# Kernel tuning notes

Measured on AMD Instinct MI355X. Metric: run time of the kernel, lower is better.

The kernel has to match this reference:

```python
import math
import jax, jax.numpy as jnp
import numpy as np

EMB_DIM = 1024
CFG_N_HEADS = 16
# Faithful to the torch module: n_heads collapses to 1 when config.n_heads < emb_dim
N_HEADS = CFG_N_HEADS if CFG_N_HEADS >= EMB_DIM else 1


def setup_inputs() -> dict:
    key = jax.random.key(0)
    ks = jax.random.split(key, 11)
    B, T, C = 4, 2048, EMB_DIM
    s = 1.0 / math.sqrt(C)
    return {
        "q": jax.random.normal(ks[0], (B, T, C), jnp.float32),
        "k": jax.random.normal(ks[1], (B, T, C), jnp.float32),
        "v": jax.random.normal(ks[2], (B, T, C), jnp.float32),
        "Wq": jax.random.normal(ks[3], (C, C), jnp.float32) * s,
        "bq": jax.random.normal(ks[4], (C,), jnp.float32) * s,
        "Wk": jax.random.normal(ks[5], (C, C), jnp.float32) * s,
        "bk": jax.random.normal(ks[6], (C,), jnp.float32) * s,
        "Wv": jax.random.normal(ks[7], (C, C), jnp.float32) * s,
        "bv": jax.random.normal(ks[8], (C,), jnp.float32) * s,
        "Wff": jax.random.normal(ks[9], (C, C), jnp.float32) * s,
        "bff": jax.random.normal(ks[10], (C,), jnp.float32) * s,
    }


def reference(q, k, v, Wq, bq, Wk, bk, Wv, bv, Wff, bff):
    B, T, C = q.shape
    H = N_HEADS
    D = C // H  # head dim (== C here since H degenerates to 1)
    # torch Linear: x @ W.T + b
    qp = (q @ Wq.T + bq).reshape(B, T, H, D).transpose(0, 2, 1, 3)  # [B,H,T,D]
    kp = (k @ Wk.T + bk).reshape(B, T, H, D).transpose(0, 2, 1, 3)
    vp = (v @ Wv.T + bv).reshape(B, T, H, D).transpose(0, 2, 1, 3)
    scale = 1.0 / math.sqrt(D)
    scores = jnp.einsum('bhqd,bhkd->bhqk', qp, kp) * scale  # [B,H,T,T]
    causal = jnp.tril(jnp.ones((T, T), dtype=bool))
    scores = jnp.where(causal[None, None, :, :], scores, -jnp.inf)
    attn = jax.nn.softmax(scores, axis=-1)
    out = jnp.einsum('bhqk,bhkd->bhqd', attn, vp)  # [B,H,T,D]
    out = out.transpose(0, 2, 1, 3).reshape(B, T, C)
    return out @ Wff.T + bff
```

## Files before the change

kernel.cpp:

```cpp
#include <hip/hip_runtime.h>
#include <stdint.h>

typedef unsigned short u16;
typedef short v8s __attribute__((ext_vector_type(8)));
typedef float v4f __attribute__((ext_vector_type(4)));

#define BM 128
#define BN 128
#define BK 32

__device__ __forceinline__ float b2f(u16 b) {
  union { unsigned u; float f; } x; x.u = ((unsigned)b) << 16; return x.f;
}
__device__ __forceinline__ u16 f2b(float f) {
  union { float f; unsigned u; } x; x.f = f;
  unsigned r = x.u + 0x7fffu + ((x.u >> 16) & 1u);
  return (u16)(r >> 16);
}

__device__ __forceinline__ void async_copy16(const void* g, void* lds) {
  __builtin_amdgcn_global_load_lds(
      (const __attribute__((address_space(1))) void*)g,
      (__attribute__((address_space(3))) void*)(uint32_t)(uintptr_t)lds,
      16, 0, 0);
}

__device__ __forceinline__ void xcd_swz(int& bx, int& by) {
  const int gx = gridDim.x;
  const int nwg = gx * gridDim.y;
  const int ord = blockIdx.y * gx + blockIdx.x;
  const int q = nwg >> 3, r = nwg & 7;
  const int xcd = ord & 7, local = ord >> 3;
  const int base = xcd < r ? xcd * (q + 1) : r * (q + 1) + (xcd - r) * q;
  const int s = base + local;
  bx = s % gx;
  by = s / gx;
}

__global__ __launch_bounds__(256) void cvt3_kernel(
    const float* __restrict__ i0, const float* __restrict__ i1,
    const float* __restrict__ i2, u16* __restrict__ o0, u16* __restrict__ o1,
    u16* __restrict__ o2, int n) {
  const int z = blockIdx.y;
  const float* in = z == 0 ? i0 : (z == 1 ? i1 : i2);
  u16* out = z == 0 ? o0 : (z == 1 ? o1 : o2);
  const int i = (blockIdx.x * 256 + threadIdx.x) * 8;
  if (i >= n) return;
  v4f a = *(const v4f*)(in + i);
  v4f b = *(const v4f*)(in + i + 4);
  v8s o;
#pragma unroll
  for (int j = 0; j < 4; j++) o[j] = (short)f2b(a[j]);
#pragma unroll
  for (int j = 0; j < 4; j++) o[4 + j] = (short)f2b(b[j]);
  *(v8s*)(out + i) = o;
}

__global__ __launch_bounds__(256) void cvt4_kernel(
    const float* __restrict__ i0, const float* __restrict__ i1,
    const float* __restrict__ i2, const float* __restrict__ i3,
    u16* __restrict__ o0, u16* __restrict__ o1, u16* __restrict__ o2,
    u16* __restrict__ o3, int n) {
  const int z = blockIdx.y;
  const float* in = z == 0 ? i0 : (z == 1 ? i1 : (z == 2 ? i2 : i3));
  u16* out = z == 0 ? o0 : (z == 1 ? o1 : (z == 2 ? o2 : o3));
  const int i = (blockIdx.x * 256 + threadIdx.x) * 8;
  if (i >= n) return;
  v4f a = *(const v4f*)(in + i);
  v4f b = *(const v4f*)(in + i + 4);
  v8s o;
#pragma unroll
  for (int j = 0; j < 4; j++) o[j] = (short)f2b(a[j]);
#pragma unroll
  for (int j = 0; j < 4; j++) o[4 + j] = (short)f2b(b[j]);
  *(v8s*)(out + i) = o;
}

template <bool HAS_BIAS, bool CAUSAL_K, bool OUT_F32>
__device__ __forceinline__ void gemm_body(
    const u16* __restrict__ A, int lda, const u16* __restrict__ Bm, int ldb,
    void* __restrict__ Cout_, int ldc, long cbase,
    const float* __restrict__ bias, int K, int m0, int n0) {
  __shared__ u16 ldsA[BM * BK];
  __shared__ u16 ldsB[BN * BK];

  const int tid = threadIdx.x;
  const int wave = tid >> 6, lane = tid & 63;
  const int wm = (wave >> 1) * 64, wn = (wave & 1) * 64;
  const int lrow = lane & 15, quad = lane >> 4;

  v4f acc[4][4];
#pragma unroll
  for (int i = 0; i < 4; i++)
#pragma unroll
    for (int j = 0; j < 4; j++) acc[i][j] = v4f{0.f, 0.f, 0.f, 0.f};

  int Keff = K;
  if (CAUSAL_K) {
    int ke = m0 + BM;
    Keff = ke < K ? ke : K;
  }

  const int r0 = tid >> 2;
  const int c0 = (tid & 3) * 8;
  const u16* pA0 = A + (long)(m0 + r0) * lda + c0;
  const u16* pA1 = A + (long)(m0 + 64 + r0) * lda + c0;
  const u16* pB0 = Bm + (long)(n0 + r0) * ldb + c0;
  const u16* pB1 = Bm + (long)(n0 + 64 + r0) * ldb + c0;
  u16* dA0 = ldsA + wave * 512;
  u16* dA1 = ldsA + 2048 + wave * 512;
  u16* dB0 = ldsB + wave * 512;
  u16* dB1 = ldsB + 2048 + wave * 512;

  for (int k0 = 0; k0 < Keff; k0 += BK) {
    async_copy16(pA0 + k0, dA0);
    async_copy16(pA1 + k0, dA1);
    async_copy16(pB0 + k0, dB0);
    async_copy16(pB1 + k0, dB1);
    __syncthreads();

    v8s af[4], bfr[4];
#pragma unroll
    for (int mt = 0; mt < 4; mt++)
      af[mt] = *(const v8s*)&ldsA[(wm + mt * 16 + lrow) * BK + quad * 8];
#pragma unroll
    for (int nt = 0; nt < 4; nt++)
      bfr[nt] = *(const v8s*)&ldsB[(wn + nt * 16 + lrow) * BK + quad * 8];
#pragma unroll
    for (int mt = 0; mt < 4; mt++)
#pragma unroll
      for (int nt = 0; nt < 4; nt++)
        acc[mt][nt] = __builtin_amdgcn_mfma_f32_16x16x32_bf16(
            af[mt], bfr[nt], acc[mt][nt], 0, 0, 0);
    __syncthreads();
  }

#pragma unroll
  for (int mt = 0; mt < 4; mt++) {
    const int rowBase = m0 + wm + mt * 16 + quad * 4;
#pragma unroll
    for (int nt = 0; nt < 4; nt++) {
      const int col = n0 + wn + nt * 16 + lrow;
      float bv = 0.f;
      if (HAS_BIAS) bv = bias[col];
#pragma unroll
      for (int i = 0; i < 4; i++) {
        const long idx = cbase + (long)(rowBase + i) * ldc + col;
        const float val = acc[mt][nt][i] + bv;
        if (OUT_F32)
          ((float*)Cout_)[idx] = val;
        else
          ((u16*)Cout_)[idx] = f2b(val);
      }
    }
  }
}

__global__ __launch_bounds__(256, 4) void qkv_gemm_kernel(
    const u16* __restrict__ a0, const u16* __restrict__ a1,
    const u16* __restrict__ a2, const u16* __restrict__ w0,
    const u16* __restrict__ w1, const u16* __restrict__ w2,
    const float* __restrict__ b0, const float* __restrict__ b1,
    const float* __restrict__ b2, u16* __restrict__ c0, u16* __restrict__ c1,
    u16* __restrict__ c2, int C) {
  const int z = blockIdx.z;
  const u16* A = z == 0 ? a0 : (z == 1 ? a1 : a2);
  const u16* W = z == 0 ? w0 : (z == 1 ? w1 : w2);
  const float* bias = z == 0 ? b0 : (z == 1 ? b1 : b2);
  u16* Cp = z == 0 ? c0 : (z == 1 ? c1 : c2);
  int bx, by;
  xcd_swz(bx, by);
  gemm_body<true, false, false>(A, C, W, C, Cp, C, 0,
                                bias, C, by * BM, bx * BN);
}

template <bool HAS_BIAS, bool CAUSAL_SKIP, bool CAUSAL_K, bool OUT_F32>
__global__ __launch_bounds__(256, 4) void gemm_bt_kernel(
    const u16* __restrict__ A, int lda, long sA,
    const u16* __restrict__ Bm, int ldb, long sB,
    void* __restrict__ Cout_, int ldc, long sC,
    const float* __restrict__ bias, int K) {
  int bx, by;
  xcd_swz(bx, by);
  const int m0 = by * BM;
  const int n0 = bx * BN;
  if (CAUSAL_SKIP && n0 > m0) return;
  const int z = blockIdx.z;
  gemm_body<HAS_BIAS, CAUSAL_K, OUT_F32>(
      A + (long)z * sA, lda, Bm + (long)z * sB, ldb, Cout_, ldc,
      (long)z * sC, bias, K, m0, n0);
}

__global__ __launch_bounds__(256) void transpose_kernel(
    const u16* __restrict__ in, u16* __restrict__ out) {
  __shared__ u16 tile[64][72];
  const int b = blockIdx.z;
  const int d0 = blockIdx.x * 64;
  const int t0 = blockIdx.y * 64;
  const u16* ip = in + (long)b * 2048 * 1024;
  u16* op = out + (long)b * 1024 * 2048;
  const int tid = threadIdx.x;
  const int tl = tid >> 2;
  const int dl = (tid & 3) * 16;
  const u16* src = ip + (long)(t0 + tl) * 1024 + d0 + dl;
  *(v8s*)&tile[tl][dl] = *(const v8s*)src;
  *(v8s*)&tile[tl][dl + 8] = *(const v8s*)(src + 8);
  __syncthreads();
  const int dd = tid >> 2;
  const int tt = (tid & 3) * 16;
  u16* dst = op + (long)(d0 + dd) * 2048 + t0 + tt;
  v8s o0, o1;
#pragma unroll
  for (int j = 0; j < 8; j++) o0[j] = (short)tile[tt + j][dd];
#pragma unroll
  for (int j = 0; j < 8; j++) o1[j] = (short)tile[tt + 8 + j][dd];
  *(v8s*)dst = o0;
  *(v8s*)(dst + 8) = o1;
}

__global__ __launch_bounds__(256) void softmax_kernel(u16* __restrict__ S) {
  const float scale = 0.03125f;
  const int i = blockIdx.x, b = blockIdx.y;
  const int tid = threadIdx.x;
  u16* row = S + ((long)b * 2048 + (long)i) * 2048;
  const int jb = tid * 8;
  const int Lw = ((i >> 7) + 1) << 7;
  v8s raw = {0, 0, 0, 0, 0, 0, 0, 0};
  if (jb <= i) raw = *(const v8s*)&row[jb];
  float v[8];
  float m = -1e30f;
#pragma unroll
  for (int jj = 0; jj < 8; jj++) {
    float x = (jb + jj <= i) ? b2f((u16)raw[jj]) * scale : -1e30f;
    v[jj] = x;
    m = fmaxf(m, x);
  }
#pragma unroll
  for (int off = 32; off; off >>= 1) m = fmaxf(m, __shfl_xor(m, off));
  __shared__ float red[4], red2[4];
  const int wave = tid >> 6, lane = tid & 63;
  if (lane == 0) red[wave] = m;
  __syncthreads();
  m = fmaxf(fmaxf(red[0], red[1]), fmaxf(red[2], red[3]));
  float s = 0.f, p[8];
#pragma unroll
  for (int jj = 0; jj < 8; jj++) {
    float e = (v[jj] > -1e29f) ? __expf(v[jj] - m) : 0.f;
    p[jj] = e;
    s += e;
  }
#pragma unroll
  for (int off = 32; off; off >>= 1) s += __shfl_xor(s, off);
  if (lane == 0) red2[wave] = s;
  __syncthreads();
  s = red2[0] + red2[1] + red2[2] + red2[3];
  const float inv = 1.0f / s;
  v8s outv;
#pragma unroll
  for (int jj = 0; jj < 8; jj++) outv[jj] = (short)f2b(p[jj] * inv);
  if (jb < Lw) *(v8s*)&row[jb] = outv;
}

extern "C" void kernel_launch(void* const* d_in, const int* in_sizes, int n_in,
                              void* d_out, int out_size, void* d_ws,
                              size_t ws_size, hipStream_t stream) {
  const float* q = (const float*)d_in[0];
  const float* k = (const float*)d_in[1];
  const float* v = (const float*)d_in[2];
  const float* Wq = (const float*)d_in[3];
  const float* bq = (const float*)d_in[4];
  const float* Wk = (const float*)d_in[5];
  const float* bk = (const float*)d_in[6];
  const float* Wv = (const float*)d_in[7];
  const float* bv = (const float*)d_in[8];
  const float* Wff = (const float*)d_in[9];
  const float* bff = (const float*)d_in[10];
  float* out = (float*)d_out;

  const int B = 4, T = 2048, C = 1024, M = B * T;
  const size_t MC = (size_t)M * C;
  const size_t CC = (size_t)C * C;
  u16* ws = (u16*)d_ws;
  u16* qb = ws;
  u16* kb = qb + MC;
  u16* vb = kb + MC;
  u16* Wqb = vb + MC;
  u16* Wkb = Wqb + CC;
  u16* Wvb = Wkb + CC;
  u16* Wffb = Wvb + CC;
  u16* Qp = Wffb + CC;
  u16* Kp = Qp + MC;
  u16* Vp = Kp + MC;
  u16* VpT = Vp + MC;
  u16* S = qb;
  u16* attn = Vp;

  dim3 blk(256);
  cvt3_kernel<<<dim3((int)(MC / 2048), 3), blk, 0, stream>>>(
      q, k, v, qb, kb, vb, (int)MC);
  cvt4_kernel<<<dim3((int)(CC / 2048), 4), blk, 0, stream>>>(
      Wq, Wk, Wv, Wff, Wqb, Wkb, Wvb, Wffb, (int)CC);

  qkv_gemm_kernel<<<dim3(C / BN, M / BM, 3), blk, 0, stream>>>(
      qb, kb, vb, Wqb, Wkb, Wvb, bq, bk, bv, Qp, Kp, Vp, C);
  transpose_kernel<<<dim3(C / 64, T / 64, B), blk, 0, stream>>>(Vp, VpT);
  gemm_bt_kernel<false, true, false, false>
      <<<dim3(T / BN, T / BM, B), blk, 0, stream>>>(
          Qp, C, (long)T * C, Kp, C, (long)T * C, S, T, (long)T * T,
          nullptr, C);
  softmax_kernel<<<dim3(T, B), blk, 0, stream>>>(S);
  gemm_bt_kernel<false, false, true, false>
      <<<dim3(C / BN, T / BM, B), blk, 0, stream>>>(
          S, T, (long)T * T, VpT, T, (long)C * T, attn, C, (long)T * C,
          nullptr, T);
  gemm_bt_kernel<true, false, false, true>
      <<<dim3(C / BN, M / BM, 1), blk, 0, stream>>>(
          attn, C, 0, Wffb, C, 0, out, C, 0, bff, C);
}
```

Measured before the change: 366.2 us.

## Double GEMM K-tile with XOR-swizzled LDS, pair causal tiles, wave-per-row softmax

Raises the GEMM K-tile from 32 to 64. The async global-to-LDS loads and the fragment reads now use an XOR-swizzled chunk layout, which halves the number of barriers per K and avoids LDS bank conflicts. The causal attention GEMMs get a block-order mapping that pairs short and long causal row blocks, to balance work across the GPU's compute dies (XCDs). Softmax now processes one row per wave instead of one per block, removing the shared-memory reductions and block barriers. The larger tile doubles LDS use per block, which may lower occupancy.

```diff
diff --git a/kernel.cpp b/kernel.cpp
--- a/kernel.cpp
+++ b/kernel.cpp
@@ -7,7 +7,7 @@
 
 #define BM 128
 #define BN 128
-#define BK 32
+#define BK 64
 
 __device__ __forceinline__ float b2f(u16 b) {
   union { unsigned u; float f; } x; x.u = ((unsigned)b) << 16; return x.f;
@@ -35,6 +35,15 @@
   const int s = base + local;
   bx = s % gx;
   by = s / gx;
+}
+
+__device__ __forceinline__ void causal_pair_swz(int& bx, int& by) {
+  const int gx = gridDim.x;
+  const int ord = blockIdx.y * gx + blockIdx.x;
+  const int k = ord & 7;
+  const int j = ord >> 3;
+  by = (j < gx) ? k : 15 - k;
+  bx = (j < gx) ? j : j - gx;
 }
 
 __global__ __launch_bounds__(256) void cvt3_kernel(
@@ -101,37 +110,43 @@
     Keff = ke < K ? ke : K;
   }
 
-  const int r0 = tid >> 2;
-  const int c0 = (tid & 3) * 8;
-  const u16* pA0 = A + (long)(m0 + r0) * lda + c0;
-  const u16* pA1 = A + (long)(m0 + 64 + r0) * lda + c0;
-  const u16* pB0 = Bm + (long)(n0 + r0) * ldb + c0;
-  const u16* pB1 = Bm + (long)(n0 + 64 + r0) * ldb + c0;
-  u16* dA0 = ldsA + wave * 512;
-  u16* dA1 = ldsA + 2048 + wave * 512;
-  u16* dB0 = ldsB + wave * 512;
-  u16* dB1 = ldsB + 2048 + wave * 512;
+  const int rA = lane >> 3;
+  const int uch = (lane & 7) ^ rA;
+  const u16* pA = A + (long)(m0 + wave * 8 + rA) * lda + uch * 8;
+  const u16* pB = Bm + (long)(n0 + wave * 8 + rA) * ldb + uch * 8;
+  u16* dA = ldsA + (wave * 8) * BK;
+  u16* dB = ldsB + (wave * 8) * BK;
 
   for (int k0 = 0; k0 < Keff; k0 += BK) {
-    async_copy16(pA0 + k0, dA0);
-    async_copy16(pA1 + k0, dA1);
-    async_copy16(pB0 + k0, dB0);
-    async_copy16(pB1 + k0, dB1);
+#pragma unroll
+    for (int c = 0; c < 4; c++) {
+      async_copy16(pA + (long)c * 32 * lda + k0, dA + c * 32 * BK);
+      async_copy16(pB + (long)c * 32 * ldb + k0, dB + c * 32 * BK);
+    }
     __syncthreads();
 
-    v8s af[4], bfr[4];
-#pragma unroll
-    for (int mt = 0; mt < 4; mt++)
-      af[mt] = *(const v8s*)&ldsA[(wm + mt * 16 + lrow) * BK + quad * 8];
-#pragma unroll
-    for (int nt = 0; nt < 4; nt++)
-      bfr[nt] = *(const v8s*)&ldsB[(wn + nt * 16 + lrow) * BK + quad * 8];
-#pragma unroll
-    for (int mt = 0; mt < 4; mt++)
-#pragma unroll
-      for (int nt = 0; nt < 4; nt++)
-        acc[mt][nt] = __builtin_amdgcn_mfma_f32_16x16x32_bf16(
-            af[mt], bfr[nt], acc[mt][nt], 0, 0, 0);
+#pragma unroll
+    for (int ks = 0; ks < 2; ks++) {
+      v8s af[4], bfr[4];
+#pragma unroll
+      for (int mt = 0; mt < 4; mt++) {
+        const int r = wm + mt * 16 + lrow;
+        af[mt] =
+            *(const v8s*)&ldsA[r * BK + ((ks * 4 + quad) ^ (r & 7)) * 8];
+      }
+#pragma unroll
+      for (int nt = 0; nt < 4; nt++) {
+        const int r = wn + nt * 16 + lrow;
+        bfr[nt] =
+            *(const v8s*)&ldsB[r * BK + ((ks * 4 + quad) ^ (r & 7)) * 8];
+      }
+#pragma unroll
+      for (int mt = 0; mt < 4; mt++)
+#pragma unroll
+        for (int nt = 0; nt < 4; nt++)
+          acc[mt][nt] = __builtin_amdgcn_mfma_f32_16x16x32_bf16(
+              af[mt], bfr[nt], acc[mt][nt], 0, 0, 0);
+    }
     __syncthreads();
   }
 
@@ -174,14 +189,18 @@
                                 bias, C, by * BM, bx * BN);
 }
 
-template <bool HAS_BIAS, bool CAUSAL_SKIP, bool CAUSAL_K, bool OUT_F32>
+template <bool HAS_BIAS, bool CAUSAL_SKIP, bool CAUSAL_K, bool OUT_F32,
+          int SWZ>
 __global__ __launch_bounds__(256, 4) void gemm_bt_kernel(
     const u16* __restrict__ A, int lda, long sA,
     const u16* __restrict__ Bm, int ldb, long sB,
     void* __restrict__ Cout_, int ldc, long sC,
     const float* __restrict__ bias, int K) {
   int bx, by;
-  xcd_swz(bx, by);
+  if (SWZ == 1)
+    causal_pair_swz(bx, by);
+  else
+    xcd_swz(bx, by);
   const int m0 = by * BM;
   const int n0 = bx * BN;
   if (CAUSAL_SKIP && n0 > m0) return;
@@ -220,45 +239,48 @@
 
 __global__ __launch_bounds__(256) void softmax_kernel(u16* __restrict__ S) {
   const float scale = 0.03125f;
-  const int i = blockIdx.x, b = blockIdx.y;
-  const int tid = threadIdx.x;
+  const int wave = threadIdx.x >> 6, lane = threadIdx.x & 63;
+  const int i = blockIdx.x * 4 + wave, b = blockIdx.y;
   u16* row = S + ((long)b * 2048 + (long)i) * 2048;
-  const int jb = tid * 8;
   const int Lw = ((i >> 7) + 1) << 7;
-  v8s raw = {0, 0, 0, 0, 0, 0, 0, 0};
-  if (jb <= i) raw = *(const v8s*)&row[jb];
-  float v[8];
+  float v[32];
   float m = -1e30f;
 #pragma unroll
-  for (int jj = 0; jj < 8; jj++) {
-    float x = (jb + jj <= i) ? b2f((u16)raw[jj]) * scale : -1e30f;
-    v[jj] = x;
-    m = fmaxf(m, x);
+  for (int c = 0; c < 4; c++) {
+    const int jb = c * 512 + lane * 8;
+    v8s raw = {0, 0, 0, 0, 0, 0, 0, 0};
+    if (jb <= i) raw = *(const v8s*)&row[jb];
+#pragma unroll
+    for (int jj = 0; jj < 8; jj++) {
+      float x = (jb + jj <= i) ? b2f((u16)raw[jj]) * scale : -1e30f;
+      v[c * 8 + jj] = x;
+      m = fmaxf(m, x);
+    }
   }
 #pragma unroll
   for (int off = 32; off; off >>= 1) m = fmaxf(m, __shfl_xor(m, off));
-  __shared__ float red[4], red2[4];
-  const int wave = tid >> 6, lane = tid & 63;
-  if (lane == 0) red[wave] = m;
-  __syncthreads();
-  m = fmaxf(fmaxf(red[0], red[1]), fmaxf(red[2], red[3]));
-  float s = 0.f, p[8];
-#pragma unroll
-  for (int jj = 0; jj < 8; jj++) {
-    float e = (v[jj] > -1e29f) ? __expf(v[jj] - m) : 0.f;
-    p[jj] = e;
-    s += e;
-  }
+  float s = 0.f;
+#pragma unroll
+  for (int c = 0; c < 4; c++)
+#pragma unroll
+    for (int jj = 0; jj < 8; jj++) {
+      float e = (v[c * 8 + jj] > -1e29f) ? __expf(v[c * 8 + jj] - m) : 0.f;
+      v[c * 8 + jj] = e;
+      s += e;
+    }
 #pragma unroll
   for (int off = 32; off; off >>= 1) s += __shfl_xor(s, off);
-  if (lane == 0) red2[wave] = s;
-  __syncthreads();
-  s = red2[0] + red2[1] + red2[2] + red2[3];
   const float inv = 1.0f / s;
-  v8s outv;
-#pragma unroll
-  for (int jj = 0; jj < 8; jj++) outv[jj] = (short)f2b(p[jj] * inv);
-  if (jb < Lw) *(v8s*)&row[jb] = outv;
+#pragma unroll
+  for (int c = 0; c < 4; c++) {
+    const int jb = c * 512 + lane * 8;
+    if (jb < Lw) {
+      v8s o;
+#pragma unroll
+      for (int jj = 0; jj < 8; jj++) o[jj] = (short)f2b(v[c * 8 + jj] * inv);
+      *(v8s*)&row[jb] = o;
+    }
+  }
 }
 
 extern "C" void kernel_launch(void* const* d_in, const int* in_sizes, int n_in,
@@ -304,16 +326,16 @@
   qkv_gemm_kernel<<<dim3(C / BN, M / BM, 3), blk, 0, stream>>>(
       qb, kb, vb, Wqb, Wkb, Wvb, bq, bk, bv, Qp, Kp, Vp, C);
   transpose_kernel<<<dim3(C / 64, T / 64, B), blk, 0, stream>>>(Vp, VpT);
-  gemm_bt_kernel<false, true, false, false>
+  gemm_bt_kernel<false, true, false, false, 1>
       <<<dim3(T / BN, T / BM, B), blk, 0, stream>>>(
           Qp, C, (long)T * C, Kp, C, (long)T * C, S, T, (long)T * T,
           nullptr, C);
-  softmax_kernel<<<dim3(T, B), blk, 0, stream>>>(S);
-  gemm_bt_kernel<false, false, true, false>
+  softmax_kernel<<<dim3(T / 4, B), blk, 0, stream>>>(S);
+  gemm_bt_kernel<false, false, true, false, 1>
       <<<dim3(C / BN, T / BM, B), blk, 0, stream>>>(
           S, T, (long)T * T, VpT, T, (long)C * T, attn, C, (long)T * C,
           nullptr, T);
-  gemm_bt_kernel<true, false, false, true>
+  gemm_bt_kernel<true, false, false, true, 0>
       <<<dim3(C / BN, M / BM, 1), blk, 0, stream>>>(
           attn, C, 0, Wffb, C, 0, out, C, 0, bff, C);
 }
```

Measured after the change: 327.9 us. -10.5%, faster.
